# Performance work log

Hardware: AMD Instinct MI355X
Metric: run time of the kernel (lower is better)

Reference implementation:

```python
import jax, jax.numpy as jnp
import numpy as np

DIM = 1024
NUM_HEADS = 16
HEAD_DIM = DIM // NUM_HEADS
MAX_LEN = 2048
ROPE_BASE = 10000.0


def _rope_tables(n, d, base=ROPE_BASE):
    inv_freq = 1.0 / (base ** (np.arange(0, d, 2, dtype=np.float32) / d))  # [d/2]
    t = np.arange(n, dtype=np.float32)
    freqs = np.outer(t, inv_freq)  # [n, d/2]
    return jnp.asarray(np.cos(freqs)), jnp.asarray(np.sin(freqs))


def _apply_rotary(x, cos, sin):
    # x: [B, H, N, D]; pairs are consecutive elements (2i, 2i+1)
    xe = x[..., 0::2]
    xo = x[..., 1::2]
    # cos/sin: [N, D/2] -> broadcast over B, H
    oe = xe * cos - xo * sin
    oo = xe * sin + xo * cos
    return jnp.stack([oe, oo], axis=-1).reshape(x.shape)


def setup_inputs() -> dict:
    key = jax.random.key(0)
    ks = jax.random.split(key, 11)
    B, T, S = 4, 2048, 2048
    sc = 1.0 / np.sqrt(DIM)
    inp = {
        "query": jax.random.normal(ks[0], (B, T, DIM), jnp.float32),
        "key": jax.random.normal(ks[1], (B, S, DIM), jnp.float32),
        "value": jax.random.normal(ks[2], (B, S, DIM), jnp.float32),
        "Wq": jax.random.normal(ks[3], (DIM, DIM), jnp.float32) * sc,
        "bq": jnp.zeros((DIM,), jnp.float32),
        "Wk": jax.random.normal(ks[4], (DIM, DIM), jnp.float32) * sc,
        "bk": jnp.zeros((DIM,), jnp.float32),
        "Wv": jax.random.normal(ks[5], (DIM, DIM), jnp.float32) * sc,
        "bv": jnp.zeros((DIM,), jnp.float32),
        "Wo": jax.random.normal(ks[6], (DIM, DIM), jnp.float32) * sc,
        "bo": jnp.zeros((DIM,), jnp.float32),
    }
    return inp


def reference(query, key, value, Wq, bq, Wk, bk, Wv, bv, Wo, bo):
    B, T, C = query.shape
    S = key.shape[1]
    H, D = NUM_HEADS, HEAD_DIM
    scale = D ** -0.5

    q = (query @ Wq + bq).reshape(B, T, H, D).transpose(0, 2, 1, 3)  # [B,H,T,D]
    k = (key @ Wk + bk).reshape(B, S, H, D).transpose(0, 2, 1, 3)    # [B,H,S,D]
    v = (value @ Wv + bv).reshape(B, S, H, D).transpose(0, 2, 1, 3)  # [B,H,S,D]

    cos, sin = _rope_tables(max(T, S), D)
    q = _apply_rotary(q, cos[:T], sin[:T])
    k = _apply_rotary(k, cos[:S], sin[:S])

    scores = jnp.einsum("bhtd,bhsd->bhts", q, k) * scale  # [B,H,T,S]
    causal = jnp.tril(jnp.ones((T, S), bool))
    scores = jnp.where(causal[None, None], scores, -jnp.inf)
    att = jax.nn.softmax(scores, axis=-1)

    out = jnp.einsum("bhts,bhsd->bhtd", att, v)  # [B,H,T,D]
    out = out.transpose(0, 2, 1, 3).reshape(B, T, C)
    return out @ Wo + bo
```

## Files before the change

kernel.cpp:

```cpp
#include <hip/hip_runtime.h>
#include <cstdint>
#include <math.h>

typedef __bf16 bf16_t;
typedef __bf16 bf16x8 __attribute__((ext_vector_type(8)));
typedef __bf16 bf16x4 __attribute__((ext_vector_type(4)));
typedef float f32x4 __attribute__((ext_vector_type(4)));

#define MFMA16(a, b, c) __builtin_amdgcn_mfma_f32_16x16x32_bf16((a), (b), (c), 0, 0, 0)

static constexpr int BATCH = 4;
static constexpr int SEQ = 2048;
static constexpr int DIMC = 1024;
static constexpr int NH = 16;
static constexpr int HD = 64;

__device__ __forceinline__ void async_copy16(void* lds, const void* g) {
    __builtin_amdgcn_global_load_lds(
        (const __attribute__((address_space(1))) void*)g,
        (__attribute__((address_space(3))) void*)lds, 16, 0, 0);
}

__device__ __forceinline__ float fast_exp2(float x) {
#if __has_builtin(__builtin_amdgcn_exp2f)
    return __builtin_amdgcn_exp2f(x);
#else
    return __expf(x * 0.6931471805599453f);
#endif
}

__global__ __launch_bounds__(256) void cvt3(const float* __restrict__ q,
                                            const float* __restrict__ k,
                                            const float* __restrict__ v,
                                            bf16_t* __restrict__ out) {
    const float* in = (blockIdx.y == 0) ? q : ((blockIdx.y == 1) ? k : v);
    bf16_t* o = out + (size_t)blockIdx.y * BATCH * SEQ * DIMC;
    const int i = blockIdx.x * 256 + threadIdx.x;
    const float4 f0 = ((const float4*)in)[i * 2];
    const float4 f1 = ((const float4*)in)[i * 2 + 1];
    bf16x8 vv;
    vv[0] = (bf16_t)f0.x; vv[1] = (bf16_t)f0.y; vv[2] = (bf16_t)f0.z; vv[3] = (bf16_t)f0.w;
    vv[4] = (bf16_t)f1.x; vv[5] = (bf16_t)f1.y; vv[6] = (bf16_t)f1.z; vv[7] = (bf16_t)f1.w;
    ((bf16x8*)o)[i] = vv;
}

__global__ __launch_bounds__(256) void transpose_cvt(const float* __restrict__ W0,
                                                     const float* __restrict__ W1,
                                                     const float* __restrict__ W2,
                                                     const float* __restrict__ W3,
                                                     bf16_t* __restrict__ out) {
    const float* Ws[4] = {W0, W1, W2, W3};
    const float* W = Ws[blockIdx.z];
    bf16_t* Wt = out + (size_t)blockIdx.z * DIMC * DIMC;
    __shared__ float tile[32][33];
    const int tx = threadIdx.x & 31;
    const int ty = threadIdx.x >> 5;
    const int x0 = blockIdx.x * 32;
    const int y0 = blockIdx.y * 32;
    #pragma unroll
    for (int j = ty; j < 32; j += 8)
        tile[j][tx] = W[(size_t)(y0 + j) * DIMC + x0 + tx];
    __syncthreads();
    #pragma unroll
    for (int j = ty; j < 32; j += 8)
        Wt[(size_t)(x0 + j) * DIMC + y0 + tx] = (bf16_t)tile[tx][j];
}

__global__ __launch_bounds__(256) void rope_tab(float* __restrict__ cosT, float* __restrict__ sinT) {
    const int idx = blockIdx.x * 256 + threadIdx.x;
    const int t = idx >> 5;
    const int p = idx & 31;
    const float inv = exp2f(-0.41524101186092029f * (float)p);
    const float ang = (float)t * inv;
    float s, c;
    sincosf(ang, &s, &c);
    cosT[idx] = c;
    sinT[idx] = s;
}

#define GEMM_KLOOP(A_, Bt_)                                                             \
    f32x4 acc[4][4] = {};                                                               \
    const int swW = ((lane >> 2) & 3) ^ ((lane >> 4) & 3);         \
    const int rIn = lane >> 2;                                    \
    const int gW = ((lane & 3) ^ swW) * 8;                        \
    const int fR = (l15 & 3) ^ ((l15 >> 2) & 3);                    \
    for (int kt = 0; kt < DIMC / 32; ++kt) {                                            \
        const int k0 = kt * 32;                                                         \
        __syncthreads();                                                                \
        _Pragma("unroll") for (int ci = 0; ci < 2; ++ci) {                              \
            const int c = 2 * w + ci;                                                   \
            async_copy16(&Bs[c * 512], Bt_ + (size_t)(col0 + c * 16 + rIn) * DIMC + k0 + gW); \
            async_copy16(&As[c * 512], A_ + (size_t)(row0 + c * 16 + rIn) * DIMC + k0 + gW);  \
        }                                                                               \
        __syncthreads();                                                                \
        bf16x8 af[4], bfr[4];                                                           \
        _Pragma("unroll") for (int mt = 0; mt < 4; ++mt)                                \
            af[mt] = *(const bf16x8*)&As[(wr * 64 + mt * 16 + l15) * 32 + ((quad ^ fR) << 3)]; \
        _Pragma("unroll") for (int nt = 0; nt < 4; ++nt)                                \
            bfr[nt] = *(const bf16x8*)&Bs[(wc * 64 + nt * 16 + l15) * 32 + ((quad ^ fR) << 3)]; \
        _Pragma("unroll") for (int mt = 0; mt < 4; ++mt)                                \
            _Pragma("unroll") for (int nt = 0; nt < 4; ++nt)                            \
                acc[mt][nt] = MFMA16(af[mt], bfr[nt], acc[mt][nt]);                     \
    }

__global__ __launch_bounds__(256) void gemm_qkv(const bf16_t* __restrict__ Cb,
                                                const bf16_t* __restrict__ Wt3,
                                                const float* __restrict__ bq,
                                                const float* __restrict__ bk,
                                                const float* __restrict__ bv,
                                                bf16_t* __restrict__ Qr,
                                                bf16_t* __restrict__ Kr,
                                                bf16_t* __restrict__ Vr,
                                                const float* __restrict__ cosT,
                                                const float* __restrict__ sinT) {
    __shared__ __align__(16) unsigned char smem[32 * 132 * 4];
    bf16_t* As = (bf16_t*)smem;
    bf16_t* Bs = (bf16_t*)(smem + 8192);
    float* eps = (float*)smem;
    const int z = blockIdx.z;
    const bf16_t* A = Cb + (size_t)z * BATCH * SEQ * DIMC;
    const bf16_t* Bt = Wt3 + (size_t)z * DIMC * DIMC;
    const float* bias = (z == 0) ? bq : ((z == 1) ? bk : bv);
    bf16_t* outp = (z == 0) ? Qr : ((z == 1) ? Kr : Vr);
    const bool rope = (z < 2);
    const int tid = threadIdx.x;
    const int w = tid >> 6;
    const int lane = tid & 63;
    const int l15 = lane & 15;
    const int quad = lane >> 4;
    const int wr = w >> 1, wc = w & 1;
    const int raw = blockIdx.y * 8 + blockIdx.x;
    const int row0 = (raw & 63) * 128, col0 = (raw >> 6) * 128;
    GEMM_KLOOP(A, Bt)
    float bvl[4];
    #pragma unroll
    for (int nt = 0; nt < 4; ++nt) bvl[nt] = bias[col0 + wc * 64 + nt * 16 + l15];
    const int lr = tid >> 3;
    const int cg = tid & 7;
    const int c0 = cg * 16;
    const int h = (col0 + c0) >> 6;
    const int dbase = (col0 + c0) & 63;
    #pragma unroll
    for (int p = 0; p < 4; ++p) {
        __syncthreads();
        #pragma unroll
        for (int nt = 0; nt < 4; ++nt)
            #pragma unroll
            for (int r = 0; r < 4; ++r)
                eps[(wr * 16 + quad * 4 + r) * 132 + wc * 64 + nt * 16 + l15] =
                    acc[p][nt][r] + bvl[nt];
        __syncthreads();
        const int grow = row0 + (lr >> 4) * 64 + p * 16 + (lr & 15);
        const int t = grow & (SEQ - 1);
        const int bb = grow >> 11;
        float vals[16];
        #pragma unroll
        for (int q4 = 0; q4 < 4; ++q4) {
            f32x4 vv = *(const f32x4*)&eps[lr * 132 + c0 + q4 * 4];
            vals[q4 * 4 + 0] = vv[0]; vals[q4 * 4 + 1] = vv[1];
            vals[q4 * 4 + 2] = vv[2]; vals[q4 * 4 + 3] = vv[3];
        }
        bf16x8 o0, o1;
        if (rope) {
            const int pbase = t * 32 + (dbase >> 1);
            const float4 cs0 = *(const float4*)&cosT[pbase];
            const float4 cs1 = *(const float4*)&cosT[pbase + 4];
            const float4 sn0 = *(const float4*)&sinT[pbase];
            const float4 sn1 = *(const float4*)&sinT[pbase + 4];
            const float cc[8] = {cs0.x, cs0.y, cs0.z, cs0.w, cs1.x, cs1.y, cs1.z, cs1.w};
            const float ss[8] = {sn0.x, sn0.y, sn0.z, sn0.w, sn1.x, sn1.y, sn1.z, sn1.w};
            #pragma unroll
            for (int i = 0; i < 8; ++i) {
                const float e = vals[2 * i], o = vals[2 * i + 1];
                const float oe = e * cc[i] - o * ss[i];
                const float oo = e * ss[i] + o * cc[i];
                if (i < 4) { o0[2 * i] = (bf16_t)oe; o0[2 * i + 1] = (bf16_t)oo; }
                else { o1[2 * (i - 4)] = (bf16_t)oe; o1[2 * (i - 4) + 1] = (bf16_t)oo; }
            }
        } else {
            #pragma unroll
            for (int i = 0; i < 8; ++i) o0[i] = (bf16_t)vals[i];
            #pragma unroll
            for (int i = 0; i < 8; ++i) o1[i] = (bf16_t)vals[8 + i];
        }
        bf16_t* dst = outp + (((size_t)bb * NH + h) * SEQ + t) * HD + dbase;
        *(bf16x8*)dst = o0;
        *(bf16x8*)(dst + 8) = o1;
    }
}

__global__ __launch_bounds__(256) void gemm_o(const bf16_t* __restrict__ A,
                                              const bf16_t* __restrict__ Bt,
                                              const float* __restrict__ bias,
                                              float* __restrict__ out) {
    __shared__ __align__(16) unsigned char smem[16384];
    bf16_t* As = (bf16_t*)smem;
    bf16_t* Bs = (bf16_t*)(smem + 8192);
    const int tid = threadIdx.x;
    const int w = tid >> 6;
    const int lane = tid & 63;
    const int l15 = lane & 15;
    const int quad = lane >> 4;
    const int wr = w >> 1, wc = w & 1;
    const int raw = blockIdx.y * 8 + blockIdx.x;
    const int row0 = (raw & 63) * 128, col0 = (raw >> 6) * 128;
    GEMM_KLOOP(A, Bt)
    #pragma unroll
    for (int nt = 0; nt < 4; ++nt) {
        const int col = col0 + wc * 64 + nt * 16 + l15;
        const float bvl = bias[col];
        #pragma unroll
        for (int mt = 0; mt < 4; ++mt) {
            #pragma unroll
            for (int r = 0; r < 4; ++r) {
                const int row = row0 + wr * 64 + mt * 16 + quad * 4 + r;
                out[(size_t)row * DIMC + col] = acc[mt][nt][r] + bvl;
            }
        }
    }
}

__global__ __launch_bounds__(256) void attn_kernel(const bf16_t* __restrict__ Qr,
                                                   const bf16_t* __restrict__ Kr,
                                                   const bf16_t* __restrict__ Vr,
                                                   bf16_t* __restrict__ O) {
    __shared__ bf16_t Ks[64 * 64];
    __shared__ bf16_t Vt[64 * 72];
    __shared__ bf16_t Ps[4][32 * 72];
    const int tid = threadIdx.x;
    const int w = tid >> 6;
    const int lane = tid & 63;
    const int l15 = lane & 15;
    const int quad = lane >> 4;
    const int bh = blockIdx.x;
    const int b = bh >> 4, h = bh & 15;
    const bf16_t* Qb = Qr + (size_t)bh * SEQ * HD;
    const bf16_t* Kb = Kr + (size_t)bh * SEQ * HD;
    const bf16_t* Vb = Vr + (size_t)bh * SEQ * HD;
    const float S2 = 0.18033688011112043f;

    bf16x8 ones;
    #pragma unroll
    for (int j8 = 0; j8 < 8; ++j8) ones[j8] = (bf16_t)1.0f;
    bf16x8 idB[2];
    #pragma unroll
    for (int ch = 0; ch < 2; ++ch)
        #pragma unroll
        for (int j8 = 0; j8 < 8; ++j8)
            idB[ch][j8] = (quad * 8 + j8 == ch * 16 + l15) ? (bf16_t)1.0f : (bf16_t)0.0f;

    const int sIn = lane >> 3;
    const int gK = ((lane & 7) ^ sIn) * 8;
    const int fK = (l15 & 7);

    for (int half = 0; half < 2; ++half) {
        const int j = (half == 0) ? blockIdx.y : 15 - blockIdx.y;
        const int q0 = j * 128;
        bf16x8 qa[2][2];
        #pragma unroll
        for (int mg = 0; mg < 2; ++mg)
            #pragma unroll
            for (int kc = 0; kc < 2; ++kc)
                qa[mg][kc] = *(const bf16x8*)(Qb + (size_t)(q0 + mg * 64 + w * 16 + l15) * HD +
                                              kc * 32 + quad * 8);
        f32x4 acco[2][4] = {};
        f32x4 accl[2] = {};
        const int nIter = 2 * j + 2;
        for (int it = 0; it < nIter; ++it) {
            const int s0 = it * 64;
            __syncthreads();
            #pragma unroll
            for (int ci = 0; ci < 2; ++ci) {
                const int c = 2 * w + ci;
                async_copy16(&Ks[c * 512], Kb + (size_t)(s0 + c * 8 + sIn) * HD + gK);
            }
            {
                const bf16_t* vsrc = Vb + (size_t)(s0 + w * 16 + l15) * HD + quad * 8;
                bf16x8 av0 = *(const bf16x8*)(vsrc);
                bf16x8 av1 = *(const bf16x8*)(vsrc + 32);
                #pragma unroll
                for (int c = 0; c < 4; ++c) {
                    f32x4 zz = {};
                    f32x4 tv = MFMA16((c < 2) ? av0 : av1, idB[c & 1], zz);
                    bf16x4 pk;
                    #pragma unroll
                    for (int r = 0; r < 4; ++r) pk[r] = (bf16_t)tv[r];
                    *(bf16x4*)&Vt[(c * 16 + l15) * 72 + w * 16 + quad * 4] = pk;
                }
            }
            __syncthreads();
            bf16x8 kb[4][2];
            #pragma unroll
            for (int mt = 0; mt < 4; ++mt)
                #pragma unroll
                for (int kc = 0; kc < 2; ++kc)
                    kb[mt][kc] = *(const bf16x8*)&Ks[(mt * 16 + l15) * 64 +
                                                     (((kc * 4 + quad) ^ fK) << 3)];
            #pragma unroll
            for (int mg = 0; mg < 2; ++mg) {
                if (mg == 0 && it == 2 * j + 1) continue;
                const bool diag = (it == 2 * j + mg);
                #pragma unroll
                for (int mt = 0; mt < 4; ++mt) {
                    f32x4 z = {};
                    z = MFMA16(kb[mt][0], qa[mg][0], z);
                    z = MFMA16(kb[mt][1], qa[mg][1], z);
                    bf16x4 pk;
                    #pragma unroll
                    for (int r = 0; r < 4; ++r) {
                        float v = z[r];
                        if (diag && (mt * 16 + quad * 4 + r > w * 16 + l15)) v = -INFINITY;
                        pk[r] = (bf16_t)fast_exp2(S2 * v);
                    }
                    *(bf16x4*)&Ps[w][(mg * 16 + l15) * 72 + mt * 16 + quad * 4] = pk;
                }
            }
            asm volatile("s_waitcnt lgkmcnt(0)" ::: "memory");
            bf16x8 vb[4][2];
            #pragma unroll
            for (int dt = 0; dt < 4; ++dt)
                #pragma unroll
                for (int kc = 0; kc < 2; ++kc)
                    vb[dt][kc] = *(const bf16x8*)&Vt[(dt * 16 + l15) * 72 + kc * 32 + quad * 8];
            #pragma unroll
            for (int mg = 0; mg < 2; ++mg) {
                if (mg == 0 && it == 2 * j + 1) continue;
                const bf16x8 pa0 = *(const bf16x8*)&Ps[w][(mg * 16 + l15) * 72 + quad * 8];
                const bf16x8 pa1 = *(const bf16x8*)&Ps[w][(mg * 16 + l15) * 72 + 32 + quad * 8];
                #pragma unroll
                for (int dt = 0; dt < 4; ++dt) {
                    acco[mg][dt] = MFMA16(pa0, vb[dt][0], acco[mg][dt]);
                    acco[mg][dt] = MFMA16(pa1, vb[dt][1], acco[mg][dt]);
                }
                accl[mg] = MFMA16(pa0, ones, accl[mg]);
                accl[mg] = MFMA16(pa1, ones, accl[mg]);
            }
        }
        #pragma unroll
        for (int mg = 0; mg < 2; ++mg) {
            #pragma unroll
            for (int r = 0; r < 4; ++r) {
                const float inv = 1.0f / accl[mg][r];
                const int trow = q0 + mg * 64 + w * 16 + quad * 4 + r;
                bf16_t* orow = O + ((size_t)(b * SEQ + trow)) * DIMC + h * HD;
                #pragma unroll
                for (int dt = 0; dt < 4; ++dt)
                    orow[dt * 16 + l15] = (bf16_t)(acco[mg][dt][r] * inv);
            }
        }
    }
}

extern "C" void kernel_launch(void* const* d_in, const int* in_sizes, int n_in,
                              void* d_out, int out_size, void* d_ws, size_t ws_size,
                              hipStream_t stream) {
    const float* query = (const float*)d_in[0];
    const float* key = (const float*)d_in[1];
    const float* value = (const float*)d_in[2];
    const float* Wq = (const float*)d_in[3];
    const float* bq = (const float*)d_in[4];
    const float* Wk = (const float*)d_in[5];
    const float* bk = (const float*)d_in[6];
    const float* Wv = (const float*)d_in[7];
    const float* bv = (const float*)d_in[8];
    const float* Wo = (const float*)d_in[9];
    const float* bo = (const float*)d_in[10];

    char* ws = (char*)d_ws;
    const size_t WT_BYTES = (size_t)DIMC * DIMC * sizeof(bf16_t);
    const size_t ACT_BYTES = (size_t)BATCH * SEQ * DIMC * sizeof(bf16_t);
    bf16_t* WT = (bf16_t*)ws;
    bf16_t* WoT = WT + 3 * (size_t)DIMC * DIMC;
    float* cosT = (float*)(ws + 4 * WT_BYTES);
    float* sinT = (float*)(ws + 4 * WT_BYTES + 262144);
    bf16_t* Cb = (bf16_t*)(ws + 4 * WT_BYTES + 2 * 262144);
    bf16_t* Qr = (bf16_t*)((char*)Cb + 3 * ACT_BYTES);
    bf16_t* Kr = (bf16_t*)((char*)Cb + 4 * ACT_BYTES);
    bf16_t* Vr = (bf16_t*)((char*)Cb + 5 * ACT_BYTES);
    bf16_t* Ob = Cb;

    transpose_cvt<<<dim3(32, 32, 4), 256, 0, stream>>>(Wq, Wk, Wv, Wo, WT);
    rope_tab<<<dim3(256), 256, 0, stream>>>(cosT, sinT);
    cvt3<<<dim3(4096, 3), 256, 0, stream>>>(query, key, value, Cb);
    gemm_qkv<<<dim3(DIMC / 128, (BATCH * SEQ) / 128, 3), 256, 0, stream>>>(
        Cb, WT, bq, bk, bv, Qr, Kr, Vr, cosT, sinT);
    attn_kernel<<<dim3(BATCH * NH, 8), 256, 0, stream>>>(Qr, Kr, Vr, Ob);
    gemm_o<<<dim3(DIMC / 128, (BATCH * SEQ) / 128), 256, 0, stream>>>(Ob, WoT, bo, (float*)d_out);
}
```

Before: 340.1 us.

## Fuse prep kernels, reschedule attention blocks, coalesce output GEMM stores

Merges the weight transpose, RoPE table and input conversion kernels into one launch, saving two launches. Attention now runs one 128-row query tile per block across 1024 blocks, ordered so heavy and light causal tiles interleave, and fully masked 16x16 sub-tiles skip their MFMAs and exp. The output GEMM stages results through shared memory so it can write coalesced float4 stores, and launch_bounds occupancy hints are added. The cost is extra LDS round trips and syncs in the epilogue, and the occupancy hints may force register spills.

After: 714.4 us. 2.1x slower.

```diff
diff --git a/kernel.cpp b/kernel.cpp
--- a/kernel.cpp
+++ b/kernel.cpp
@@ -29,53 +29,62 @@
 #endif
 }
 
-__global__ __launch_bounds__(256) void cvt3(const float* __restrict__ q,
+__global__ __launch_bounds__(256) void prep(const float* __restrict__ Wq,
+                                            const float* __restrict__ Wk,
+                                            const float* __restrict__ Wv,
+                                            const float* __restrict__ Wo,
+                                            const float* __restrict__ q,
                                             const float* __restrict__ k,
                                             const float* __restrict__ v,
-                                            bf16_t* __restrict__ out) {
-    const float* in = (blockIdx.y == 0) ? q : ((blockIdx.y == 1) ? k : v);
-    bf16_t* o = out + (size_t)blockIdx.y * BATCH * SEQ * DIMC;
-    const int i = blockIdx.x * 256 + threadIdx.x;
-    const float4 f0 = ((const float4*)in)[i * 2];
-    const float4 f1 = ((const float4*)in)[i * 2 + 1];
-    bf16x8 vv;
-    vv[0] = (bf16_t)f0.x; vv[1] = (bf16_t)f0.y; vv[2] = (bf16_t)f0.z; vv[3] = (bf16_t)f0.w;
-    vv[4] = (bf16_t)f1.x; vv[5] = (bf16_t)f1.y; vv[6] = (bf16_t)f1.z; vv[7] = (bf16_t)f1.w;
-    ((bf16x8*)o)[i] = vv;
-}
-
-__global__ __launch_bounds__(256) void transpose_cvt(const float* __restrict__ W0,
-                                                     const float* __restrict__ W1,
-                                                     const float* __restrict__ W2,
-                                                     const float* __restrict__ W3,
-                                                     bf16_t* __restrict__ out) {
-    const float* Ws[4] = {W0, W1, W2, W3};
-    const float* W = Ws[blockIdx.z];
-    bf16_t* Wt = out + (size_t)blockIdx.z * DIMC * DIMC;
+                                            bf16_t* __restrict__ WT,
+                                            float* __restrict__ cosT,
+                                            float* __restrict__ sinT,
+                                            bf16_t* __restrict__ Cb) {
     __shared__ float tile[32][33];
-    const int tx = threadIdx.x & 31;
-    const int ty = threadIdx.x >> 5;
-    const int x0 = blockIdx.x * 32;
-    const int y0 = blockIdx.y * 32;
-    #pragma unroll
-    for (int j = ty; j < 32; j += 8)
-        tile[j][tx] = W[(size_t)(y0 + j) * DIMC + x0 + tx];
-    __syncthreads();
-    #pragma unroll
-    for (int j = ty; j < 32; j += 8)
-        Wt[(size_t)(x0 + j) * DIMC + y0 + tx] = (bf16_t)tile[tx][j];
-}
-
-__global__ __launch_bounds__(256) void rope_tab(float* __restrict__ cosT, float* __restrict__ sinT) {
-    const int idx = blockIdx.x * 256 + threadIdx.x;
-    const int t = idx >> 5;
-    const int p = idx & 31;
-    const float inv = exp2f(-0.41524101186092029f * (float)p);
-    const float ang = (float)t * inv;
-    float s, c;
-    sincosf(ang, &s, &c);
-    cosT[idx] = c;
-    sinT[idx] = s;
+    const int n = blockIdx.x;
+    const int tid = threadIdx.x;
+    if (n < 4096) {
+        const int z = n >> 10;
+        const int yx = n & 1023;
+        const int by = yx >> 5, bx = yx & 31;
+        const float* Ws[4] = {Wq, Wk, Wv, Wo};
+        const float* W = Ws[z];
+        bf16_t* Wt = WT + (size_t)z * DIMC * DIMC;
+        const int tx = tid & 31;
+        const int ty = tid >> 5;
+        const int x0 = bx * 32;
+        const int y0 = by * 32;
+        #pragma unroll
+        for (int jj = ty; jj < 32; jj += 8)
+            tile[jj][tx] = W[(size_t)(y0 + jj) * DIMC + x0 + tx];
+        __syncthreads();
+        #pragma unroll
+        for (int jj = ty; jj < 32; jj += 8)
+            Wt[(size_t)(x0 + jj) * DIMC + y0 + tx] = (bf16_t)tile[tx][jj];
+    } else if (n < 4352) {
+        const int idx = (n - 4096) * 256 + tid;
+        const int t = idx >> 5;
+        const int p = idx & 31;
+        const float inv = exp2f(-0.41524101186092029f * (float)p);
+        const float ang = (float)t * inv;
+        float s, c;
+        sincosf(ang, &s, &c);
+        cosT[idx] = c;
+        sinT[idx] = s;
+    } else {
+        const int m = n - 4352;
+        const int y = m >> 12;
+        const int x = m & 4095;
+        const float* in = (y == 0) ? q : ((y == 1) ? k : v);
+        bf16_t* o = Cb + (size_t)y * BATCH * SEQ * DIMC;
+        const int i = x * 256 + tid;
+        const float4 f0 = ((const float4*)in)[i * 2];
+        const float4 f1 = ((const float4*)in)[i * 2 + 1];
+        bf16x8 vv;
+        vv[0] = (bf16_t)f0.x; vv[1] = (bf16_t)f0.y; vv[2] = (bf16_t)f0.z; vv[3] = (bf16_t)f0.w;
+        vv[4] = (bf16_t)f1.x; vv[5] = (bf16_t)f1.y; vv[6] = (bf16_t)f1.z; vv[7] = (bf16_t)f1.w;
+        ((bf16x8*)o)[i] = vv;
+    }
 }
 
 #define GEMM_KLOOP(A_, Bt_)                                                             \
@@ -103,16 +112,16 @@
                 acc[mt][nt] = MFMA16(af[mt], bfr[nt], acc[mt][nt]);                     \
     }
 
-__global__ __launch_bounds__(256) void gemm_qkv(const bf16_t* __restrict__ Cb,
-                                                const bf16_t* __restrict__ Wt3,
-                                                const float* __restrict__ bq,
-                                                const float* __restrict__ bk,
-                                                const float* __restrict__ bv,
-                                                bf16_t* __restrict__ Qr,
-                                                bf16_t* __restrict__ Kr,
-                                                bf16_t* __restrict__ Vr,
-                                                const float* __restrict__ cosT,
-                                                const float* __restrict__ sinT) {
+__global__ __launch_bounds__(256, 6) void gemm_qkv(const bf16_t* __restrict__ Cb,
+                                                   const bf16_t* __restrict__ Wt3,
+                                                   const float* __restrict__ bq,
+                                                   const float* __restrict__ bk,
+                                                   const float* __restrict__ bv,
+                                                   bf16_t* __restrict__ Qr,
+                                                   bf16_t* __restrict__ Kr,
+                                                   bf16_t* __restrict__ Vr,
+                                                   const float* __restrict__ cosT,
+                                                   const float* __restrict__ sinT) {
     __shared__ __align__(16) unsigned char smem[32 * 132 * 4];
     bf16_t* As = (bf16_t*)smem;
     bf16_t* Bs = (bf16_t*)(smem + 8192);
@@ -189,13 +198,14 @@
     }
 }
 
-__global__ __launch_bounds__(256) void gemm_o(const bf16_t* __restrict__ A,
-                                              const bf16_t* __restrict__ Bt,
-                                              const float* __restrict__ bias,
-                                              float* __restrict__ out) {
-    __shared__ __align__(16) unsigned char smem[16384];
+__global__ __launch_bounds__(256, 6) void gemm_o(const bf16_t* __restrict__ A,
+                                                 const bf16_t* __restrict__ Bt,
+                                                 const float* __restrict__ bias,
+                                                 float* __restrict__ out) {
+    __shared__ __align__(16) unsigned char smem[32 * 132 * 4];
     bf16_t* As = (bf16_t*)smem;
     bf16_t* Bs = (bf16_t*)(smem + 8192);
+    float* eps = (float*)smem;
     const int tid = threadIdx.x;
     const int w = tid >> 6;
     const int lane = tid & 63;
@@ -205,25 +215,35 @@
     const int raw = blockIdx.y * 8 + blockIdx.x;
     const int row0 = (raw & 63) * 128, col0 = (raw >> 6) * 128;
     GEMM_KLOOP(A, Bt)
-    #pragma unroll
-    for (int nt = 0; nt < 4; ++nt) {
-        const int col = col0 + wc * 64 + nt * 16 + l15;
-        const float bvl = bias[col];
-        #pragma unroll
-        for (int mt = 0; mt < 4; ++mt) {
-            #pragma unroll
-            for (int r = 0; r < 4; ++r) {
-                const int row = row0 + wr * 64 + mt * 16 + quad * 4 + r;
-                out[(size_t)row * DIMC + col] = acc[mt][nt][r] + bvl;
-            }
-        }
-    }
-}
-
-__global__ __launch_bounds__(256) void attn_kernel(const bf16_t* __restrict__ Qr,
-                                                   const bf16_t* __restrict__ Kr,
-                                                   const bf16_t* __restrict__ Vr,
-                                                   bf16_t* __restrict__ O) {
+    float bvl[4];
+    #pragma unroll
+    for (int nt = 0; nt < 4; ++nt) bvl[nt] = bias[col0 + wc * 64 + nt * 16 + l15];
+    const int lr = tid >> 3;
+    const int cg = tid & 7;
+    #pragma unroll
+    for (int p = 0; p < 4; ++p) {
+        __syncthreads();
+        #pragma unroll
+        for (int nt = 0; nt < 4; ++nt)
+            #pragma unroll
+            for (int r = 0; r < 4; ++r)
+                eps[(wr * 16 + quad * 4 + r) * 132 + wc * 64 + nt * 16 + l15] =
+                    acc[p][nt][r] + bvl[nt];
+        __syncthreads();
+        const int grow = row0 + (lr >> 4) * 64 + p * 16 + (lr & 15);
+        float* dst = out + (size_t)grow * DIMC + col0 + cg * 16;
+        #pragma unroll
+        for (int q4 = 0; q4 < 4; ++q4) {
+            f32x4 vv = *(const f32x4*)&eps[lr * 132 + cg * 16 + q4 * 4];
+            *(f32x4*)(dst + q4 * 4) = vv;
+        }
+    }
+}
+
+__global__ __launch_bounds__(256, 4) void attn_kernel(const bf16_t* __restrict__ Qr,
+                                                      const bf16_t* __restrict__ Kr,
+                                                      const bf16_t* __restrict__ Vr,
+                                                      bf16_t* __restrict__ O) {
     __shared__ bf16_t Ks[64 * 64];
     __shared__ bf16_t Vt[64 * 72];
     __shared__ bf16_t Ps[4][32 * 72];
@@ -232,7 +252,12 @@
     const int lane = tid & 63;
     const int l15 = lane & 15;
     const int quad = lane >> 4;
-    const int bh = blockIdx.x;
+    const int n = blockIdx.x;
+    const int rnd = n >> 8;
+    const int c255 = n & 255;
+    const int bh = c255 & 63;
+    const int base = c255 >> 6;
+    const int j = (rnd == 0) ? base : (rnd == 1) ? (7 - base) : (rnd == 2) ? (8 + base) : (15 - base);
     const int b = bh >> 4, h = bh & 15;
     const bf16_t* Qb = Qr + (size_t)bh * SEQ * HD;
     const bf16_t* Kb = Kr + (size_t)bh * SEQ * HD;
@@ -253,100 +278,102 @@
     const int gK = ((lane & 7) ^ sIn) * 8;
     const int fK = (l15 & 7);
 
-    for (int half = 0; half < 2; ++half) {
-        const int j = (half == 0) ? blockIdx.y : 15 - blockIdx.y;
-        const int q0 = j * 128;
-        bf16x8 qa[2][2];
-        #pragma unroll
-        for (int mg = 0; mg < 2; ++mg)
+    const int q0 = j * 128;
+    bf16x8 qa[2][2];
+    #pragma unroll
+    for (int mg = 0; mg < 2; ++mg)
+        #pragma unroll
+        for (int kc = 0; kc < 2; ++kc)
+            qa[mg][kc] = *(const bf16x8*)(Qb + (size_t)(q0 + mg * 64 + w * 16 + l15) * HD +
+                                          kc * 32 + quad * 8);
+    f32x4 acco[2][4] = {};
+    f32x4 accl[2] = {};
+    const int nIter = 2 * j + 2;
+    for (int it = 0; it < nIter; ++it) {
+        const int s0 = it * 64;
+        __syncthreads();
+        #pragma unroll
+        for (int ci = 0; ci < 2; ++ci) {
+            const int c = 2 * w + ci;
+            async_copy16(&Ks[c * 512], Kb + (size_t)(s0 + c * 8 + sIn) * HD + gK);
+        }
+        {
+            const bf16_t* vsrc = Vb + (size_t)(s0 + w * 16 + l15) * HD + quad * 8;
+            bf16x8 av0 = *(const bf16x8*)(vsrc);
+            bf16x8 av1 = *(const bf16x8*)(vsrc + 32);
+            #pragma unroll
+            for (int c = 0; c < 4; ++c) {
+                f32x4 zz = {};
+                f32x4 tv = MFMA16((c < 2) ? av0 : av1, idB[c & 1], zz);
+                bf16x4 pk;
+                #pragma unroll
+                for (int r = 0; r < 4; ++r) pk[r] = (bf16_t)tv[r];
+                *(bf16x4*)&Vt[(c * 16 + l15) * 72 + w * 16 + quad * 4] = pk;
+            }
+        }
+        __syncthreads();
+        bf16x8 kb[4][2];
+        #pragma unroll
+        for (int mt = 0; mt < 4; ++mt)
             #pragma unroll
             for (int kc = 0; kc < 2; ++kc)
-                qa[mg][kc] = *(const bf16x8*)(Qb + (size_t)(q0 + mg * 64 + w * 16 + l15) * HD +
-                                              kc * 32 + quad * 8);
-        f32x4 acco[2][4] = {};
-        f32x4 accl[2] = {};
-        const int nIter = 2 * j + 2;
-        for (int it = 0; it < nIter; ++it) {
-            const int s0 = it * 64;
-            __syncthreads();
-            #pragma unroll
-            for (int ci = 0; ci < 2; ++ci) {
-                const int c = 2 * w + ci;
-                async_copy16(&Ks[c * 512], Kb + (size_t)(s0 + c * 8 + sIn) * HD + gK);
-            }
-            {
-                const bf16_t* vsrc = Vb + (size_t)(s0 + w * 16 + l15) * HD + quad * 8;
-                bf16x8 av0 = *(const bf16x8*)(vsrc);
-                bf16x8 av1 = *(const bf16x8*)(vsrc + 32);
-                #pragma unroll
-                for (int c = 0; c < 4; ++c) {
-                    f32x4 zz = {};
-                    f32x4 tv = MFMA16((c < 2) ? av0 : av1, idB[c & 1], zz);
-                    bf16x4 pk;
+                kb[mt][kc] = *(const bf16x8*)&Ks[(mt * 16 + l15) * 64 +
+                                                 (((kc * 4 + quad) ^ fK) << 3)];
+        #pragma unroll
+        for (int mg = 0; mg < 2; ++mg) {
+            if (mg == 0 && it == 2 * j + 1) continue;
+            const bool diag = (it == 2 * j + mg);
+            #pragma unroll
+            for (int mt = 0; mt < 4; ++mt) {
+                bf16x4 pk;
+                if (diag && mt > w) {
                     #pragma unroll
-                    for (int r = 0; r < 4; ++r) pk[r] = (bf16_t)tv[r];
-                    *(bf16x4*)&Vt[(c * 16 + l15) * 72 + w * 16 + quad * 4] = pk;
-                }
-            }
-            __syncthreads();
-            bf16x8 kb[4][2];
-            #pragma unroll
-            for (int mt = 0; mt < 4; ++mt)
-                #pragma unroll
-                for (int kc = 0; kc < 2; ++kc)
-                    kb[mt][kc] = *(const bf16x8*)&Ks[(mt * 16 + l15) * 64 +
-                                                     (((kc * 4 + quad) ^ fK) << 3)];
-            #pragma unroll
-            for (int mg = 0; mg < 2; ++mg) {
-                if (mg == 0 && it == 2 * j + 1) continue;
-                const bool diag = (it == 2 * j + mg);
-                #pragma unroll
-                for (int mt = 0; mt < 4; ++mt) {
+                    for (int r = 0; r < 4; ++r) pk[r] = (bf16_t)0.0f;
+                } else {
                     f32x4 z = {};
                     z = MFMA16(kb[mt][0], qa[mg][0], z);
                     z = MFMA16(kb[mt][1], qa[mg][1], z);
-                    bf16x4 pk;
                     #pragma unroll
                     for (int r = 0; r < 4; ++r) {
                         float v = z[r];
                         if (diag && (mt * 16 + quad * 4 + r > w * 16 + l15)) v = -INFINITY;
                         pk[r] = (bf16_t)fast_exp2(S2 * v);
                     }
-                    *(bf16x4*)&Ps[w][(mg * 16 + l15) * 72 + mt * 16 + quad * 4] = pk;
                 }
+                *(bf16x4*)&Ps[w][(mg * 16 + l15) * 72 + mt * 16 + quad * 4] = pk;
             }
-            asm volatile("s_waitcnt lgkmcnt(0)" ::: "memory");
-            bf16x8 vb[4][2];
+        }
+        asm volatile("s_waitcnt lgkmcnt(0)" ::: "memory");
+        bf16x8 vb[4][2];
+        #pragma unroll
+        for (int dt = 0; dt < 4; ++dt)
+            #pragma unroll
+            for (int kc = 0; kc < 2; ++kc)
+                vb[dt][kc] = *(const bf16x8*)&Vt[(dt * 16 + l15) * 72 + kc * 32 + quad * 8];
+        #pragma unroll
+        for (int mg = 0; mg < 2; ++mg) {
+            if (mg == 0 && it == 2 * j + 1) continue;
+            const bf16x8 pa0 = *(const bf16x8*)&Ps[w][(mg * 16 + l15) * 72 + quad * 8];
+            const bf16x8 pa1 = *(const bf16x8*)&Ps[w][(mg * 16 + l15) * 72 + 32 + quad * 8];
+            #pragma unroll
+            for (int dt = 0; dt < 4; ++dt) {
+                acco[mg][dt] = MFMA16(pa0, vb[dt][0], acco[mg][dt]);
+                acco[mg][dt] = MFMA16(pa1, vb[dt][1], acco[mg][dt]);
+            }
+            accl[mg] = MFMA16(pa0, ones, accl[mg]);
+            accl[mg] = MFMA16(pa1, ones, accl[mg]);
+        }
+    }
+    #pragma unroll
+    for (int mg = 0; mg < 2; ++mg) {
+        #pragma unroll
+        for (int r = 0; r < 4; ++r) {
+            const float inv = 1.0f / accl[mg][r];
+            const int trow = q0 + mg * 64 + w * 16 + quad * 4 + r;
+            bf16_t* orow = O + ((size_t)(b * SEQ + trow)) * DIMC + h * HD;
             #pragma unroll
             for (int dt = 0; dt < 4; ++dt)
-                #pragma unroll
-                for (int kc = 0; kc < 2; ++kc)
-                    vb[dt][kc] = *(const bf16x8*)&Vt[(dt * 16 + l15) * 72 + kc * 32 + quad * 8];
-            #pragma unroll
-            for (int mg = 0; mg < 2; ++mg) {
-                if (mg == 0 && it == 2 * j + 1) continue;
-                const bf16x8 pa0 = *(const bf16x8*)&Ps[w][(mg * 16 + l15) * 72 + quad * 8];
-                const bf16x8 pa1 = *(const bf16x8*)&Ps[w][(mg * 16 + l15) * 72 + 32 + quad * 8];
-                #pragma unroll
-                for (int dt = 0; dt < 4; ++dt) {
-                    acco[mg][dt] = MFMA16(pa0, vb[dt][0], acco[mg][dt]);
-                    acco[mg][dt] = MFMA16(pa1, vb[dt][1], acco[mg][dt]);
-                }
-                accl[mg] = MFMA16(pa0, ones, accl[mg]);
-                accl[mg] = MFMA16(pa1, ones, accl[mg]);
-            }
-        }
-        #pragma unroll
-        for (int mg = 0; mg < 2; ++mg) {
-            #pragma unroll
-            for (int r = 0; r < 4; ++r) {
-                const float inv = 1.0f / accl[mg][r];
-                const int trow = q0 + mg * 64 + w * 16 + quad * 4 + r;
-                bf16_t* orow = O + ((size_t)(b * SEQ + trow)) * DIMC + h * HD;
-                #pragma unroll
-                for (int dt = 0; dt < 4; ++dt)
-                    orow[dt * 16 + l15] = (bf16_t)(acco[mg][dt][r] * inv);
-            }
+                orow[dt * 16 + l15] = (bf16_t)(acco[mg][dt][r] * inv);
         }
     }
 }
@@ -379,11 +406,10 @@
     bf16_t* Vr = (bf16_t*)((char*)Cb + 5 * ACT_BYTES);
     bf16_t* Ob = Cb;
 
-    transpose_cvt<<<dim3(32, 32, 4), 256, 0, stream>>>(Wq, Wk, Wv, Wo, WT);
-    rope_tab<<<dim3(256), 256, 0, stream>>>(cosT, sinT);
-    cvt3<<<dim3(4096, 3), 256, 0, stream>>>(query, key, value, Cb);
+    prep<<<dim3(16640), 256, 0, stream>>>(Wq, Wk, Wv, Wo, query, key, value,
+                                          WT, cosT, sinT, Cb);
     gemm_qkv<<<dim3(DIMC / 128, (BATCH * SEQ) / 128, 3), 256, 0, stream>>>(
         Cb, WT, bq, bk, bv, Qr, Kr, Vr, cosT, sinT);
-    attn_kernel<<<dim3(BATCH * NH, 8), 256, 0, stream>>>(Qr, Kr, Vr, Ob);
+    attn_kernel<<<dim3(1024), 256, 0, stream>>>(Qr, Kr, Vr, Ob);
     gemm_o<<<dim3(DIMC / 128, (BATCH * SEQ) / 128), 256, 0, stream>>>(Ob, WoT, bo, (float*)d_out);
 }
```
